# Optimization experiments

Measured on AMD Instinct MI355X. Metric: run time of the kernel, lower is better.

Reference implementation:

```python
import jax, jax.numpy as jnp
import numpy as np

B, S, HID = 2, 2048, 1024
NH, HD = 4, 256
SCALE = HD ** -0.5


def _rope(x, fr, fi):
    # x: [B,S,NH,HD]; fr/fi: [S,HD//2]
    b, s, n, d = x.shape
    xr = x.reshape(b, s, n, d // 2, 2)
    re, im = xr[..., 0], xr[..., 1]
    fr = fr[None, :, None, :]
    fi = fi[None, :, None, :]
    rr = re * fr - im * fi
    ri = re * fi + im * fr
    return jnp.stack((rr, ri), axis=-1).reshape(b, s, n, d)


def setup_inputs() -> dict:
    key = jax.random.key(0)
    k1, k2, k3 = jax.random.split(key, 3)
    hidden_states = jax.random.normal(k1, (B, S, HID), dtype=jnp.float32)
    # RoPE frequencies (standard theta=10000)
    inv_freq = 1.0 / (10000.0 ** (np.arange(0, HD, 2, dtype=np.float32) / HD))  # [HD//2]
    t = np.arange(S, dtype=np.float32)
    ang = np.outer(t, inv_freq)  # [S, HD//2]
    freqs_real = jnp.asarray(np.cos(ang), dtype=jnp.float32)
    freqs_imag = jnp.asarray(np.sin(ang), dtype=jnp.float32)
    # causal additive mask [1,1,S,S]
    causal = jnp.tril(jnp.ones((S, S), dtype=bool))
    mask = jnp.where(causal, 0.0, -1e9).astype(jnp.float32)[None, None]
    W_qkv = jax.random.normal(k2, (3 * HID, HID), dtype=jnp.float32) * (HID ** -0.5)
    W_o = jax.random.normal(k3, (HID, HID), dtype=jnp.float32) * (HID ** -0.5)
    return {"hidden_states": hidden_states, "freqs_real": freqs_real,
            "freqs_imag": freqs_imag, "mask": mask, "W_qkv": W_qkv, "W_o": W_o}


def reference(hidden_states, freqs_real, freqs_imag, mask, W_qkv, W_o):
    b, s, _ = hidden_states.shape
    qkv = hidden_states @ W_qkv.T  # [B,S,3*HID]
    qkv = qkv.reshape(b, s, 3, NH, HD)
    q, k, v = qkv[:, :, 0], qkv[:, :, 1], qkv[:, :, 2]
    q = _rope(q, freqs_real, freqs_imag)
    k = _rope(k, freqs_real, freqs_imag)
    scores = jnp.einsum('bqhd,bkhd->bhqk', q * SCALE, k) + mask  # [B,NH,S,S]
    probs = jax.nn.softmax(scores, axis=-1)
    attn = jnp.einsum('bhqk,bkhd->bqhd', probs, v).reshape(b, s, HID)
    return attn @ W_o.T
```

## Files before the change

kernel.cpp:

```cpp
#include <hip/hip_runtime.h>
#include <stdint.h>

#define NB 2
#define NS 2048
#define NHID 1024
#define NHEADS 4
#define DHEAD 256
#define NP 128
#define QK_SCALE 0.0625f

typedef unsigned short ushort_t;
typedef __bf16 bf16x8 __attribute__((ext_vector_type(8)));
typedef float floatx4 __attribute__((ext_vector_type(4)));
typedef short shortx8 __attribute__((ext_vector_type(8)));
typedef unsigned short ushortx4 __attribute__((ext_vector_type(4)));
typedef unsigned short ushortx8 __attribute__((ext_vector_type(8)));

__device__ __forceinline__ float bf2f(ushort_t u) {
    unsigned int x = ((unsigned int)u) << 16;
    return __builtin_bit_cast(float, x);
}
__device__ __forceinline__ ushort_t f2bf(float f) {
    unsigned int u = __builtin_bit_cast(unsigned int, f);
    u += 0x7fff + ((u >> 16) & 1);
    return (ushort_t)(u >> 16);
}

__device__ __forceinline__ floatx4 mfma16(bf16x8 a, bf16x8 b, floatx4 c) {
    return __builtin_amdgcn_mfma_f32_16x16x32_bf16(a, b, c, 0, 0, 0);
}

__device__ __forceinline__ void gload_lds16(const void* g, void* l) {
    __builtin_amdgcn_global_load_lds(
        (const __attribute__((address_space(1))) void*)g,
        (__attribute__((address_space(3))) void*)l, 16, 0, 0);
}

#define QWAITV0  do { asm volatile("s_waitcnt vmcnt(0)" ::: "memory"); \
                      __builtin_amdgcn_sched_barrier(0); } while (0)
#define QWAITV8  do { asm volatile("s_waitcnt vmcnt(8)" ::: "memory"); \
                      __builtin_amdgcn_sched_barrier(0); } while (0)
#define QWAITL   do { asm volatile("s_waitcnt lgkmcnt(0)" ::: "memory"); \
                      __builtin_amdgcn_sched_barrier(0); } while (0)
#define QBAR     do { asm volatile("" ::: "memory"); \
                      __builtin_amdgcn_s_barrier(); \
                      asm volatile("" ::: "memory"); } while (0)

#define N4_H (4096 * 1024 / 4)
#define N4_WQ (3072 * 1024 / 4)
#define N4_WO (1024 * 1024 / 4)
__global__ __launch_bounds__(256) void cast3_kernel(const float* __restrict__ inH,
                                                    const float* __restrict__ inWq,
                                                    const float* __restrict__ inWo,
                                                    ushort_t* __restrict__ out) {
    int i = blockIdx.x * 256 + threadIdx.x;
    const float* src;
    int j = i;
    if (i < N4_H) {
        src = inH;
    } else if (i < N4_H + N4_WQ) {
        src = inWq; j = i - N4_H;
    } else {
        src = inWo; j = i - (N4_H + N4_WQ);
    }
    float4 v = ((const float4*)src)[j];
    ushortx4 o = { f2bf(v.x), f2bf(v.y), f2bf(v.z), f2bf(v.w) };
    ((ushortx4*)out)[i] = o;
}

__global__ __launch_bounds__(256, 2) void gemm_bt_f32s(const ushort_t* __restrict__ A,
                                                       const ushort_t* __restrict__ Bt,
                                                       float* __restrict__ C,
                                                       int M, int N, int K) {
    __shared__ ushort_t sA[2][8192];
    __shared__ ushort_t sB[2][4096];
    const int t = threadIdx.x;
    const int f = blockIdx.x;
    const int xcd = f & 7;
    const int idx = f >> 3;
    const int m0 = (xcd * 4 + (idx & 3)) * 128;
    const int n0 = (idx >> 2) * 64;
    const int w = t >> 6, l = t & 63;
    const int wr = w >> 1, wc = w & 1;
    const int wrm = wr * 64, wcn = wc * 32;
    const int lc = l & 15, lq = l >> 4;

    floatx4 acc[4][2];
#pragma unroll
    for (int i = 0; i < 4; i++)
#pragma unroll
        for (int j = 0; j < 2; j++) acc[i][j] = (floatx4){0.f, 0.f, 0.f, 0.f};

    const int arow = t >> 3;
    const int ac8 = ((((t & 7) - (arow & 7)) & 7)) * 8;
    const ushort_t* Ab = A + (size_t)(m0 + arow) * K + ac8;
    const ushort_t* Bb = Bt + (size_t)(n0 + arow) * K + ac8;
    const int ldst = t * 8;

    auto STAGE_A = [&](int buf, int kk) {
#pragma unroll
        for (int is = 0; is < 4; is++)
            gload_lds16(Ab + (size_t)(is * 32) * K + kk, &sA[buf][is * 2048 + ldst]);
    };
    auto STAGE_B = [&](int buf, int kk) {
#pragma unroll
        for (int is = 0; is < 2; is++)
            gload_lds16(Bb + (size_t)(is * 32) * K + kk, &sB[buf][is * 2048 + ldst]);
    };

    STAGE_A(0, 0); STAGE_B(0, 0);

#pragma unroll 1
    for (int kt = 0; kt < 16; ++kt) {
        const int b = kt & 1, nb = b ^ 1;
        const int kn = (kt + 1) * 64;
        const ushort_t* cA = sA[b];
        const ushort_t* cB = sB[b];
        bf16x8 af[4][2], bfr[2][2];

        QWAITV0;
        QBAR;
#pragma unroll
        for (int ii = 0; ii < 4; ii++) {
            const int R = wrm + ii * 16 + lc;
            af[ii][0] = *(const bf16x8*)&cA[R * 64 + ((lq + R) & 7) * 8];
            af[ii][1] = *(const bf16x8*)&cA[R * 64 + ((4 + lq + R) & 7) * 8];
        }
#pragma unroll
        for (int jj = 0; jj < 2; jj++) {
            const int R = wcn + jj * 16 + lc;
            bfr[jj][0] = *(const bf16x8*)&cB[R * 64 + ((lq + R) & 7) * 8];
            bfr[jj][1] = *(const bf16x8*)&cB[R * 64 + ((4 + lq + R) & 7) * 8];
        }
        if (kt < 15) { STAGE_A(nb, kn); STAGE_B(nb, kn); }
        QWAITL;
        __builtin_amdgcn_s_setprio(1);
#pragma unroll
        for (int ii = 0; ii < 4; ii++)
#pragma unroll
            for (int jj = 0; jj < 2; jj++) {
                acc[ii][jj] = mfma16(af[ii][0], bfr[jj][0], acc[ii][jj]);
                acc[ii][jj] = mfma16(af[ii][1], bfr[jj][1], acc[ii][jj]);
            }
        __builtin_amdgcn_s_setprio(0);
    }

#pragma unroll
    for (int i = 0; i < 4; i++) {
        int row = m0 + wrm + i * 16 + lq * 4;
#pragma unroll
        for (int j = 0; j < 2; j++) {
            int col = n0 + wcn + j * 16 + lc;
#pragma unroll
            for (int r = 0; r < 4; r++)
                C[(size_t)(row + r) * N + col] = acc[i][j][r];
        }
    }
}

__global__ __launch_bounds__(512, 2) void gemm_qkv(const ushort_t* __restrict__ A,
                                                   const ushort_t* __restrict__ Bt,
                                                   const float* __restrict__ fre,
                                                   const float* __restrict__ fim,
                                                   ushort_t* __restrict__ Q,
                                                   ushort_t* __restrict__ Kk,
                                                   ushort_t* __restrict__ Vt) {
    __shared__ ushort_t sA[2][16384];
    __shared__ ushort_t sB[2][12288];
    const int t = threadIdx.x;
    const int f = blockIdx.x;
    const int xcd = f & 7;
    const int idx = f >> 3;
    const int mreg = xcd >> 1, nreg = xcd & 1;
    const int im = idx & 3, in = idx >> 2;
    const int m0 = (mreg * 4 + im) * 256;
    const int n0 = (nreg * 8 + in) * 192;
    const int w = t >> 6, l = t & 63;
    const int wr = w >> 2, wc = w & 3;
    const int wrm = wr * 128, wcn = wc * 48;
    const int lc = l & 15, lq = l >> 4;

    floatx4 acc[8][3];
#pragma unroll
    for (int i = 0; i < 8; i++)
#pragma unroll
        for (int j = 0; j < 3; j++) acc[i][j] = (floatx4){0.f, 0.f, 0.f, 0.f};

    const int arow = t >> 3;
    const int ac8 = ((((t & 7) - (arow & 7)) & 7)) * 8;
    const ushort_t* Ab = A + (size_t)(m0 + arow) * 1024 + ac8;
    const ushort_t* Bb = Bt + (size_t)(n0 + arow) * 1024 + ac8;
    const int ldst = t * 8;

    auto STAGE_A2 = [&](int buf, int half, int kk) {
        gload_lds16(Ab + (size_t)(half * 128) * 1024 + kk, &sA[buf][half * 8192 + ldst]);
        gload_lds16(Ab + (size_t)(half * 128 + 64) * 1024 + kk, &sA[buf][half * 8192 + 4096 + ldst]);
    };
    auto STAGE_B3 = [&](int buf, int kk) {
        gload_lds16(Bb + kk, &sB[buf][ldst]);
        gload_lds16(Bb + (size_t)64 * 1024 + kk, &sB[buf][4096 + ldst]);
        gload_lds16(Bb + (size_t)128 * 1024 + kk, &sB[buf][8192 + ldst]);
    };

    STAGE_A2(0, 0, 0); STAGE_A2(0, 1, 0); STAGE_B3(0, 0);

#pragma unroll 1
    for (int kt = 0; kt < 16; ++kt) {
        const int b = kt & 1, nb = b ^ 1;
        const int kn = (kt + 1) * 64;
        const ushort_t* cA = sA[b];
        const ushort_t* cB = sB[b];
        bf16x8 af[4][2], bfr[3][2];

        QWAITV0;
        QBAR;
#pragma unroll
        for (int ii = 0; ii < 4; ii++) {
            const int R = wrm + ii * 16 + lc;
            af[ii][0] = *(const bf16x8*)&cA[R * 64 + ((lq + R) & 7) * 8];
            af[ii][1] = *(const bf16x8*)&cA[R * 64 + ((4 + lq + R) & 7) * 8];
        }
#pragma unroll
        for (int jj = 0; jj < 2; jj++) {
            const int R = wcn + jj * 16 + lc;
            bfr[jj][0] = *(const bf16x8*)&cB[R * 64 + ((lq + R) & 7) * 8];
            bfr[jj][1] = *(const bf16x8*)&cB[R * 64 + ((4 + lq + R) & 7) * 8];
        }
        if (kt < 15) STAGE_A2(nb, 0, kn);
        QWAITL;
        __builtin_amdgcn_s_setprio(1);
#pragma unroll
        for (int ii = 0; ii < 4; ii++)
#pragma unroll
            for (int jj = 0; jj < 2; jj++) {
                acc[ii][jj] = mfma16(af[ii][0], bfr[jj][0], acc[ii][jj]);
                acc[ii][jj] = mfma16(af[ii][1], bfr[jj][1], acc[ii][jj]);
            }
        __builtin_amdgcn_s_setprio(0);

        QBAR;
        {
            const int R = wcn + 32 + lc;
            bfr[2][0] = *(const bf16x8*)&cB[R * 64 + ((lq + R) & 7) * 8];
            bfr[2][1] = *(const bf16x8*)&cB[R * 64 + ((4 + lq + R) & 7) * 8];
        }
        if (kt < 15) STAGE_A2(nb, 1, kn);
        QWAITL;
        __builtin_amdgcn_s_setprio(1);
#pragma unroll
        for (int ii = 0; ii < 4; ii++) {
            acc[ii][2] = mfma16(af[ii][0], bfr[2][0], acc[ii][2]);
            acc[ii][2] = mfma16(af[ii][1], bfr[2][1], acc[ii][2]);
        }
        __builtin_amdgcn_s_setprio(0);

        QBAR;
#pragma unroll
        for (int ii = 0; ii < 4; ii++) {
            const int R = wrm + 64 + ii * 16 + lc;
            af[ii][0] = *(const bf16x8*)&cA[R * 64 + ((lq + R) & 7) * 8];
            af[ii][1] = *(const bf16x8*)&cA[R * 64 + ((4 + lq + R) & 7) * 8];
        }
        if (kt < 15) STAGE_B3(nb, kn);
        QWAITL;
        __builtin_amdgcn_s_setprio(1);
#pragma unroll
        for (int ii = 0; ii < 4; ii++) {
            acc[4 + ii][2] = mfma16(af[ii][0], bfr[2][0], acc[4 + ii][2]);
            acc[4 + ii][2] = mfma16(af[ii][1], bfr[2][1], acc[4 + ii][2]);
        }
        __builtin_amdgcn_s_setprio(0);

        QBAR;
#pragma unroll
        for (int jj = 0; jj < 2; jj++) {
            const int R = wcn + jj * 16 + lc;
            bfr[jj][0] = *(const bf16x8*)&cB[R * 64 + ((lq + R) & 7) * 8];
            bfr[jj][1] = *(const bf16x8*)&cB[R * 64 + ((4 + lq + R) & 7) * 8];
        }
        QWAITL;
        __builtin_amdgcn_s_setprio(1);
#pragma unroll
        for (int ii = 0; ii < 4; ii++)
#pragma unroll
            for (int jj = 0; jj < 2; jj++) {
                acc[4 + ii][jj] = mfma16(af[ii][0], bfr[jj][0], acc[4 + ii][jj]);
                acc[4 + ii][jj] = mfma16(af[ii][1], bfr[jj][1], acc[4 + ii][jj]);
            }
        __builtin_amdgcn_s_setprio(0);
    }

#pragma unroll
    for (int i = 0; i < 8; i++) {
        int row = m0 + wrm + i * 16 + lq * 4;
        int bb = row >> 11;
        int srow2 = row & 2047;
#pragma unroll
        for (int j = 0; j < 3; j++) {
            int c0 = n0 + wcn + j * 16;
            int sect = c0 >> 10;
            int h = (c0 >> 8) & 3;
            int d = (c0 & 255) + lc;
            int bh = bb * NHEADS + h;
            if (sect == 2) {
                ushortx4 pack = { f2bf(acc[i][j][0]), f2bf(acc[i][j][1]),
                                  f2bf(acc[i][j][2]), f2bf(acc[i][j][3]) };
                *(ushortx4*)&Vt[((size_t)bh * 256 + d) * NS + srow2] = pack;
            } else {
                int p = d >> 1;
                int odd = d & 1;
                ushort_t* dst = (sect == 0) ? Q : Kk;
#pragma unroll
                for (int r = 0; r < 4; r++) {
                    float v = acc[i][j][r];
                    float vp = __shfl_xor(v, 1);
                    int s = srow2 + r;
                    float c = fre[s * NP + p], si = fim[s * NP + p];
                    float out = odd ? (vp * si + v * c) : (v * c - vp * si);
                    if (sect == 0) out *= QK_SCALE;
                    dst[((size_t)bh * NS + s) * DHEAD + d] = f2bf(out);
                }
            }
        }
    }
}

#define BQ3 128
#define BKV3 64
#define PPAD 72
#define CHCAP 6
#define NPART_BH 51
#define OPART_SPLIT 224

__global__ __launch_bounds__(256, 2) void flash_attn4(const ushort_t* __restrict__ Q,
                                                      const ushort_t* __restrict__ K,
                                                      const ushort_t* __restrict__ Vt,
                                                      ushort_t* __restrict__ OpA,
                                                      ushort_t* __restrict__ OpB,
                                                      float* __restrict__ ml) {
    __shared__ ushort_t sK[BKV3 * 256];
    __shared__ ushort_t sV[DHEAD * 64];
    __shared__ ushort_t sP[4][16 * PPAD];

    int rem = blockIdx.x, qt = 15, nsp;
    for (;;) {
        nsp = (2 * (qt + 1) + CHCAP - 1) / CHCAP;
        if (rem < nsp) break;
        rem -= nsp;
        qt--;
    }
    const int nch = 2 * (qt + 1);
    const int cbeg = rem * CHCAP;
    const int cend = (cbeg + CHCAP < nch) ? cbeg + CHCAP : nch;

    const int h = blockIdx.y, b = blockIdx.z;
    const int t = threadIdx.x, w = t >> 6, l = t & 63;
    const int lc = l & 15, lq = l >> 4;
    const int bh = b * NHEADS + h;
    const size_t base = (size_t)bh * NS * DHEAD;
    const int q0 = qt * BQ3;

    const int krb = w * 2 + (l >> 5);
    const int kck = ((l & 31) - (krb & 7)) & 31;
    const size_t koff = (size_t)krb * 256 + kck * 8;
    const int vrb = w * 8 + (l >> 3);
    const int vck = ((l & 7) - (vrb & 7)) & 7;
    const size_t voff = (size_t)vrb * NS + vck * 8;
    ushort_t* dK = &sK[w * 512 + l * 8];
    ushort_t* dV = &sV[w * 512 + l * 8];

    bf16x8 qf[2][8];
#pragma unroll
    for (int gq = 0; gq < 2; gq++) {
        const ushort_t* qrow = Q + base + (size_t)(q0 + w * 32 + gq * 16 + lc) * DHEAD + lq * 8;
#pragma unroll
        for (int dk = 0; dk < 8; dk++) qf[gq][dk] = *(const bf16x8*)(qrow + dk * 32);
    }

    floatx4 accO[2][16];
#pragma unroll
    for (int gq = 0; gq < 2; gq++)
#pragma unroll
        for (int j = 0; j < 16; j++) accO[gq][j] = (floatx4){0.f, 0.f, 0.f, 0.f};
    float lrun[2][4] = {{0.f, 0.f, 0.f, 0.f}, {0.f, 0.f, 0.f, 0.f}};

    for (int kc = cbeg; kc < cend; kc++) {
        const int kb = kc * BKV3;
        __syncthreads();
        {
            const ushort_t* ksrc = K + base + (size_t)kb * 256 + koff;
            const ushort_t* vsrc = Vt + base + kb + voff;
#pragma unroll
            for (int j = 0; j < 8; j++)
                gload_lds16(ksrc + j * (8 * 256), dK + j * 2048);
#pragma unroll
            for (int j = 0; j < 8; j++)
                gload_lds16(vsrc + j * (32 * NS), dV + j * 2048);
        }
        QWAITV8;
        QBAR;

        floatx4 sfr[2][4];
#pragma unroll
        for (int gq = 0; gq < 2; gq++)
#pragma unroll
            for (int g = 0; g < 4; g++) sfr[gq][g] = (floatx4){0.f, 0.f, 0.f, 0.f};
#pragma unroll
        for (int dk = 0; dk < 8; dk++) {
#pragma unroll
            for (int g = 0; g < 4; g++) {
                int R = g * 16 + lc;
                int phys = (dk * 4 + lq + (R & 7)) & 31;
                bf16x8 bk = *(const bf16x8*)&sK[R * 256 + phys * 8];
                sfr[0][g] = mfma16(qf[0][dk], bk, sfr[0][g]);
                sfr[1][g] = mfma16(qf[1][dk], bk, sfr[1][g]);
            }
        }

        if (kc >= nch - 2) {
#pragma unroll
            for (int gq = 0; gq < 2; gq++)
#pragma unroll
                for (int g = 0; g < 4; g++) {
                    int kg = kb + g * 16 + lc;
                    int qr = q0 + w * 32 + gq * 16 + lq * 4;
#pragma unroll
                    for (int r = 0; r < 4; r++)
                        if (kg > qr + r) sfr[gq][g][r] = -1e30f;
                }
        }

        QWAITV0;
        QBAR;

        ushort_t* pw = sP[w];
#pragma unroll
        for (int gq = 0; gq < 2; gq++) {
#pragma unroll
            for (int g = 0; g < 4; g++)
#pragma unroll
                for (int r = 0; r < 4; r++) {
                    float p = __expf(sfr[gq][g][r]);
                    lrun[gq][r] += p;
                    pw[(lq * 4 + r) * PPAD + g * 16 + lc] = f2bf(p);
                }
            bf16x8 ap0 = *(const bf16x8*)&pw[lc * PPAD + lq * 8];
            bf16x8 ap1 = *(const bf16x8*)&pw[lc * PPAD + 32 + lq * 8];
#pragma unroll
            for (int j = 0; j < 16; j++) {
                int D = j * 16 + lc;
                int ph0 = (lq + (D & 7)) & 7;
                int ph1 = (4 + lq + (D & 7)) & 7;
                bf16x8 bv0 = *(const bf16x8*)&sV[D * 64 + ph0 * 8];
                bf16x8 bv1 = *(const bf16x8*)&sV[D * 64 + ph1 * 8];
                accO[gq][j] = mfma16(ap0, bv0, accO[gq][j]);
                accO[gq][j] = mfma16(ap1, bv1, accO[gq][j]);
            }
        }
    }

    const int pid = bh * NPART_BH + blockIdx.x;
    ushort_t* op = (pid < OPART_SPLIT) ? OpA + (size_t)pid * (128 * 256)
                                       : OpB + (size_t)(pid - OPART_SPLIT) * (128 * 256);
#pragma unroll
    for (int gq = 0; gq < 2; gq++) {
#pragma unroll
        for (int r = 0; r < 4; r++) {
            int row = w * 32 + gq * 16 + lq * 4 + r;
#pragma unroll
            for (int j = 0; j < 16; j++)
                op[row * 256 + j * 16 + lc] = f2bf(accO[gq][j][r]);
            float lv = lrun[gq][r];
#pragma unroll
            for (int off = 1; off < 16; off <<= 1) lv += __shfl_xor(lv, off);
            if (lc == 0) ml[(size_t)pid * 128 + row] = lv;
        }
    }
}

__global__ __launch_bounds__(256) void combine_parts2(const ushort_t* __restrict__ OpA,
                                                      const ushort_t* __restrict__ OpB,
                                                      const float* __restrict__ ml,
                                                      ushort_t* __restrict__ O) {
    const int qt = blockIdx.x >> 3, rsub = blockIdx.x & 7;
    const int h = blockIdx.y, b = blockIdx.z;
    const int bh = b * NHEADS + h;
    int bbase = 0;
    for (int q = 15; q > qt; q--) bbase += (2 * (q + 1) + CHCAP - 1) / CHCAP;
    const int nsp = (2 * (qt + 1) + CHCAP - 1) / CHCAP;
    const int pid0 = bh * NPART_BH + bbase;

    const int t = threadIdx.x;
    const int rl = t >> 4;
    const int c0 = (t & 15) * 16;
    const int row = rsub * 16 + rl;

    float so[16];
#pragma unroll
    for (int k = 0; k < 16; k++) so[k] = 0.f;
    float sl = 0.f;

    for (int i = 0; i < nsp; i++) {
        int pid = pid0 + i;
        const ushort_t* op = (pid < OPART_SPLIT)
                                 ? OpA + (size_t)pid * (128 * 256)
                                 : OpB + (size_t)(pid - OPART_SPLIT) * (128 * 256);
        const ushort_t* p = op + row * 256 + c0;
        ushortx8 a0 = *(const ushortx8*)p;
        ushortx8 a1 = *(const ushortx8*)(p + 8);
#pragma unroll
        for (int k = 0; k < 8; k++) {
            so[k] += bf2f(a0[k]);
            so[8 + k] += bf2f(a1[k]);
        }
        sl += ml[(size_t)pid * 128 + row];
    }

    float inv = 1.f / sl;
    ushortx8 o0, o1;
#pragma unroll
    for (int k = 0; k < 8; k++) {
        o0[k] = f2bf(so[k] * inv);
        o1[k] = f2bf(so[8 + k] * inv);
    }
    int s = qt * BQ3 + row;
    ushort_t* dst = O + ((size_t)(b * NS + s) * NHEADS + h) * DHEAD + c0;
    *(ushortx8*)dst = o0;
    *(ushortx8*)(dst + 8) = o1;
}

extern "C" void kernel_launch(void* const* d_in, const int* in_sizes, int n_in,
                              void* d_out, int out_size, void* d_ws, size_t ws_size,
                              hipStream_t stream) {
    const float* hidden = (const float*)d_in[0];
    const float* fre = (const float*)d_in[1];
    const float* fim = (const float*)d_in[2];
    const float* Wqkv = (const float*)d_in[4];
    const float* Wo = (const float*)d_in[5];

    char* ws = (char*)d_ws;
    ushort_t* hb    = (ushort_t*)(ws);
    ushort_t* wqkvb = (ushort_t*)(ws + 8388608);
    ushort_t* wob   = (ushort_t*)(ws + 14680064);
    ushort_t* qb    = (ushort_t*)(ws + 16777216);
    ushort_t* kb    = (ushort_t*)(ws + 25165824);
    ushort_t* vtb   = (ushort_t*)(ws + 33554432);
    ushort_t* OpA   = (ushort_t*)(ws);
    ushort_t* OpB   = (ushort_t*)(ws + 41943040);
    ushort_t* oattn = (ushort_t*)(ws + 16777216);
    float*    ml    = (float*)(ws + 58720256);

    cast3_kernel<<<(N4_H + N4_WQ + N4_WO) / 256, 256, 0, stream>>>(hidden, Wqkv, Wo, hb);

    gemm_qkv<<<dim3(256), 512, 0, stream>>>(
        hb, wqkvb, fre, fim, qb, kb, vtb);

    flash_attn4<<<dim3(NPART_BH, NHEADS, NB), 256, 0, stream>>>(qb, kb, vtb, OpA, OpB, ml);
    combine_parts2<<<dim3(128, NHEADS, NB), 256, 0, stream>>>(OpA, OpB, ml, oattn);

    gemm_bt_f32s<<<dim3(512), 256, 0, stream>>>(
        oattn, wob, (float*)d_out, 4096, 1024, 1024);
}
```

Before: 191.0 us.

## Triple-buffer GEMM LDS staging and prefetch next K tile in attention loop

The bf16 GEMM moves from double to triple LDS buffering, issuing loads two K-tiles ahead and waiting with a partial vmcnt so global loads overlap more MFMA work. The attention kernel issues the first K tile before the loop, then prefetches the next chunk's K into LDS right after the QK^T phase, overlapping that load with softmax and PV. This adds LDS footprint in the GEMM, which may reduce occupancy, and relies on exact vmcnt accounting and barrier placement for correctness.

```diff
diff --git a/kernel.cpp b/kernel.cpp
--- a/kernel.cpp
+++ b/kernel.cpp
@@ -37,6 +37,8 @@
 }
 
 #define QWAITV0  do { asm volatile("s_waitcnt vmcnt(0)" ::: "memory"); \
+                      __builtin_amdgcn_sched_barrier(0); } while (0)
+#define QWAITV6  do { asm volatile("s_waitcnt vmcnt(6)" ::: "memory"); \
                       __builtin_amdgcn_sched_barrier(0); } while (0)
 #define QWAITV8  do { asm volatile("s_waitcnt vmcnt(8)" ::: "memory"); \
                       __builtin_amdgcn_sched_barrier(0); } while (0)
@@ -72,8 +74,8 @@
                                                        const ushort_t* __restrict__ Bt,
                                                        float* __restrict__ C,
                                                        int M, int N, int K) {
-    __shared__ ushort_t sA[2][8192];
-    __shared__ ushort_t sB[2][4096];
+    __shared__ ushort_t sA[3][8192];
+    __shared__ ushort_t sB[3][4096];
     const int t = threadIdx.x;
     const int f = blockIdx.x;
     const int xcd = f & 7;
@@ -97,29 +99,18 @@
     const ushort_t* Bb = Bt + (size_t)(n0 + arow) * K + ac8;
     const int ldst = t * 8;
 
-    auto STAGE_A = [&](int buf, int kk) {
+    auto STAGE = [&](int buf, int kk) {
 #pragma unroll
         for (int is = 0; is < 4; is++)
             gload_lds16(Ab + (size_t)(is * 32) * K + kk, &sA[buf][is * 2048 + ldst]);
-    };
-    auto STAGE_B = [&](int buf, int kk) {
 #pragma unroll
         for (int is = 0; is < 2; is++)
             gload_lds16(Bb + (size_t)(is * 32) * K + kk, &sB[buf][is * 2048 + ldst]);
     };
-
-    STAGE_A(0, 0); STAGE_B(0, 0);
-
-#pragma unroll 1
-    for (int kt = 0; kt < 16; ++kt) {
-        const int b = kt & 1, nb = b ^ 1;
-        const int kn = (kt + 1) * 64;
-        const ushort_t* cA = sA[b];
-        const ushort_t* cB = sB[b];
+    auto COMPUTE = [&](int buf) {
+        const ushort_t* cA = sA[buf];
+        const ushort_t* cB = sB[buf];
         bf16x8 af[4][2], bfr[2][2];
-
-        QWAITV0;
-        QBAR;
 #pragma unroll
         for (int ii = 0; ii < 4; ii++) {
             const int R = wrm + ii * 16 + lc;
@@ -132,7 +123,6 @@
             bfr[jj][0] = *(const bf16x8*)&cB[R * 64 + ((lq + R) & 7) * 8];
             bfr[jj][1] = *(const bf16x8*)&cB[R * 64 + ((4 + lq + R) & 7) * 8];
         }
-        if (kt < 15) { STAGE_A(nb, kn); STAGE_B(nb, kn); }
         QWAITL;
         __builtin_amdgcn_s_setprio(1);
 #pragma unroll
@@ -143,7 +133,21 @@
                 acc[ii][jj] = mfma16(af[ii][1], bfr[jj][1], acc[ii][jj]);
             }
         __builtin_amdgcn_s_setprio(0);
-    }
+    };
+
+    STAGE(0, 0); STAGE(1, 64);
+
+#pragma unroll 1
+    for (int kt = 0; kt < 15; ++kt) {
+        QWAITV6;
+        QBAR;
+        const int cb = kt % 3;
+        if (kt < 14) STAGE((kt + 2) % 3, (kt + 2) * 64);
+        COMPUTE(cb);
+    }
+    QWAITV0;
+    QBAR;
+    COMPUTE(15 % 3);
 
 #pragma unroll
     for (int i = 0; i < 4; i++) {
@@ -376,6 +380,14 @@
 #pragma unroll
         for (int dk = 0; dk < 8; dk++) qf[gq][dk] = *(const bf16x8*)(qrow + dk * 32);
     }
+    QWAITV0;
+
+    {
+        const ushort_t* ksrc0 = K + base + (size_t)(cbeg * BKV3) * 256 + koff;
+#pragma unroll
+        for (int j = 0; j < 8; j++)
+            gload_lds16(ksrc0 + j * (8 * 256), dK + j * 2048);
+    }
 
     floatx4 accO[2][16];
 #pragma unroll
@@ -386,13 +398,10 @@
 
     for (int kc = cbeg; kc < cend; kc++) {
         const int kb = kc * BKV3;
-        __syncthreads();
+
+        QBAR;
         {
-            const ushort_t* ksrc = K + base + (size_t)kb * 256 + koff;
             const ushort_t* vsrc = Vt + base + kb + voff;
-#pragma unroll
-            for (int j = 0; j < 8; j++)
-                gload_lds16(ksrc + j * (8 * 256), dK + j * 2048);
 #pragma unroll
             for (int j = 0; j < 8; j++)
                 gload_lds16(vsrc + j * (32 * NS), dV + j * 2048);
@@ -430,7 +439,16 @@
                 }
         }
 
-        QWAITV0;
+        QBAR;
+        if (kc + 1 < cend) {
+            const ushort_t* ksrc = K + base + (size_t)((kc + 1) * BKV3) * 256 + koff;
+#pragma unroll
+            for (int j = 0; j < 8; j++)
+                gload_lds16(ksrc + j * (8 * 256), dK + j * 2048);
+            QWAITV8;
+        } else {
+            QWAITV0;
+        }
         QBAR;
 
         ushort_t* pw = sP[w];
```

New measurement: 196.5 us. +2.9%, slower.

## Shrink QKV GEMM tile to 128x192 and double grid to 512 blocks

Applied to the files above, without the earlier changes.

Halves the M tile of the fused QKV GEMM from 256 to 128 rows, which halves the A shared-memory buffer and the accumulator registers. The grid doubles to 512 blocks, the XCD-to-tile mapping changes, and launch bounds allow 4 blocks per CU. The four-phase interleaved staging/compute schedule becomes a single load-all-then-compute phase per k-step. The aim is more occupancy and better CU coverage, at the cost of lower arithmetic intensity (more global traffic per FLOP) and less overlap inside each k-step.

```diff
diff --git a/kernel.cpp b/kernel.cpp
--- a/kernel.cpp
+++ b/kernel.cpp
@@ -158,31 +158,31 @@
     }
 }
 
-__global__ __launch_bounds__(512, 2) void gemm_qkv(const ushort_t* __restrict__ A,
+__global__ __launch_bounds__(512, 4) void gemm_qkv(const ushort_t* __restrict__ A,
                                                    const ushort_t* __restrict__ Bt,
                                                    const float* __restrict__ fre,
                                                    const float* __restrict__ fim,
                                                    ushort_t* __restrict__ Q,
                                                    ushort_t* __restrict__ Kk,
                                                    ushort_t* __restrict__ Vt) {
-    __shared__ ushort_t sA[2][16384];
+    __shared__ ushort_t sA[2][8192];
     __shared__ ushort_t sB[2][12288];
     const int t = threadIdx.x;
     const int f = blockIdx.x;
     const int xcd = f & 7;
     const int idx = f >> 3;
-    const int mreg = xcd >> 1, nreg = xcd & 1;
-    const int im = idx & 3, in = idx >> 2;
-    const int m0 = (mreg * 4 + im) * 256;
+    const int mreg = xcd & 3, nreg = xcd >> 2;
+    const int im = idx & 7, in = idx >> 3;
+    const int m0 = (mreg * 8 + im) * 128;
     const int n0 = (nreg * 8 + in) * 192;
     const int w = t >> 6, l = t & 63;
     const int wr = w >> 2, wc = w & 3;
-    const int wrm = wr * 128, wcn = wc * 48;
+    const int wrm = wr * 64, wcn = wc * 48;
     const int lc = l & 15, lq = l >> 4;
 
-    floatx4 acc[8][3];
-#pragma unroll
-    for (int i = 0; i < 8; i++)
+    floatx4 acc[4][3];
+#pragma unroll
+    for (int i = 0; i < 4; i++)
 #pragma unroll
         for (int j = 0; j < 3; j++) acc[i][j] = (floatx4){0.f, 0.f, 0.f, 0.f};
 
@@ -192,17 +192,15 @@
     const ushort_t* Bb = Bt + (size_t)(n0 + arow) * 1024 + ac8;
     const int ldst = t * 8;
 
-    auto STAGE_A2 = [&](int buf, int half, int kk) {
-        gload_lds16(Ab + (size_t)(half * 128) * 1024 + kk, &sA[buf][half * 8192 + ldst]);
-        gload_lds16(Ab + (size_t)(half * 128 + 64) * 1024 + kk, &sA[buf][half * 8192 + 4096 + ldst]);
-    };
-    auto STAGE_B3 = [&](int buf, int kk) {
+    auto STAGE = [&](int buf, int kk) {
+        gload_lds16(Ab + kk, &sA[buf][ldst]);
+        gload_lds16(Ab + (size_t)64 * 1024 + kk, &sA[buf][4096 + ldst]);
         gload_lds16(Bb + kk, &sB[buf][ldst]);
         gload_lds16(Bb + (size_t)64 * 1024 + kk, &sB[buf][4096 + ldst]);
         gload_lds16(Bb + (size_t)128 * 1024 + kk, &sB[buf][8192 + ldst]);
     };
 
-    STAGE_A2(0, 0, 0); STAGE_A2(0, 1, 0); STAGE_B3(0, 0);
+    STAGE(0, 0);
 
 #pragma unroll 1
     for (int kt = 0; kt < 16; ++kt) {
@@ -221,77 +219,26 @@
             af[ii][1] = *(const bf16x8*)&cA[R * 64 + ((4 + lq + R) & 7) * 8];
         }
 #pragma unroll
-        for (int jj = 0; jj < 2; jj++) {
+        for (int jj = 0; jj < 3; jj++) {
             const int R = wcn + jj * 16 + lc;
             bfr[jj][0] = *(const bf16x8*)&cB[R * 64 + ((lq + R) & 7) * 8];
             bfr[jj][1] = *(const bf16x8*)&cB[R * 64 + ((4 + lq + R) & 7) * 8];
         }
-        if (kt < 15) STAGE_A2(nb, 0, kn);
+        if (kt < 15) STAGE(nb, kn);
         QWAITL;
         __builtin_amdgcn_s_setprio(1);
 #pragma unroll
         for (int ii = 0; ii < 4; ii++)
 #pragma unroll
-            for (int jj = 0; jj < 2; jj++) {
+            for (int jj = 0; jj < 3; jj++) {
                 acc[ii][jj] = mfma16(af[ii][0], bfr[jj][0], acc[ii][jj]);
                 acc[ii][jj] = mfma16(af[ii][1], bfr[jj][1], acc[ii][jj]);
             }
         __builtin_amdgcn_s_setprio(0);
-
-        QBAR;
-        {
-            const int R = wcn + 32 + lc;
-            bfr[2][0] = *(const bf16x8*)&cB[R * 64 + ((lq + R) & 7) * 8];
-            bfr[2][1] = *(const bf16x8*)&cB[R * 64 + ((4 + lq + R) & 7) * 8];
-        }
-        if (kt < 15) STAGE_A2(nb, 1, kn);
-        QWAITL;
-        __builtin_amdgcn_s_setprio(1);
-#pragma unroll
-        for (int ii = 0; ii < 4; ii++) {
-            acc[ii][2] = mfma16(af[ii][0], bfr[2][0], acc[ii][2]);
-            acc[ii][2] = mfma16(af[ii][1], bfr[2][1], acc[ii][2]);
-        }
-        __builtin_amdgcn_s_setprio(0);
-
-        QBAR;
-#pragma unroll
-        for (int ii = 0; ii < 4; ii++) {
-            const int R = wrm + 64 + ii * 16 + lc;
-            af[ii][0] = *(const bf16x8*)&cA[R * 64 + ((lq + R) & 7) * 8];
-            af[ii][1] = *(const bf16x8*)&cA[R * 64 + ((4 + lq + R) & 7) * 8];
-        }
-        if (kt < 15) STAGE_B3(nb, kn);
-        QWAITL;
-        __builtin_amdgcn_s_setprio(1);
-#pragma unroll
-        for (int ii = 0; ii < 4; ii++) {
-            acc[4 + ii][2] = mfma16(af[ii][0], bfr[2][0], acc[4 + ii][2]);
-            acc[4 + ii][2] = mfma16(af[ii][1], bfr[2][1], acc[4 + ii][2]);
-        }
-        __builtin_amdgcn_s_setprio(0);
-
-        QBAR;
-#pragma unroll
-        for (int jj = 0; jj < 2; jj++) {
-            const int R = wcn + jj * 16 + lc;
-            bfr[jj][0] = *(const bf16x8*)&cB[R * 64 + ((lq + R) & 7) * 8];
-            bfr[jj][1] = *(const bf16x8*)&cB[R * 64 + ((4 + lq + R) & 7) * 8];
-        }
-        QWAITL;
-        __builtin_amdgcn_s_setprio(1);
-#pragma unroll
-        for (int ii = 0; ii < 4; ii++)
-#pragma unroll
-            for (int jj = 0; jj < 2; jj++) {
-                acc[4 + ii][jj] = mfma16(af[ii][0], bfr[jj][0], acc[4 + ii][jj]);
-                acc[4 + ii][jj] = mfma16(af[ii][1], bfr[jj][1], acc[4 + ii][jj]);
-            }
-        __builtin_amdgcn_s_setprio(0);
-    }
-
-#pragma unroll
-    for (int i = 0; i < 8; i++) {
+    }
+
+#pragma unroll
+    for (int i = 0; i < 4; i++) {
         int row = m0 + wrm + i * 16 + lq * 4;
         int bb = row >> 11;
         int srow2 = row & 2047;
@@ -552,7 +499,7 @@
 
     cast3_kernel<<<(N4_H + N4_WQ + N4_WO) / 256, 256, 0, stream>>>(hidden, Wqkv, Wo, hb);
 
-    gemm_qkv<<<dim3(256), 512, 0, stream>>>(
+    gemm_qkv<<<dim3(512), 512, 0, stream>>>(
         hb, wqkvb, fre, fim, qb, kb, vtb);
 
     flash_attn4<<<dim3(NPART_BH, NHEADS, NB), 256, 0, stream>>>(qb, kb, vtb, OpA, OpB, ml);
```

Measured after the change: 181.5 us. 5.0% less time.
